# Performance work log

Hardware: AMD Instinct MI355X
Metric: run time of the kernel (lower is better)

## Reference

```python
import jax, jax.numpy as jnp
import numpy as np

NUM_GROUPS = 8
MEAN_DEGREE = 32.0
MAX_NUM_ITER = 10
NUM_NODES = 50000
NUM_UND_EDGES = 800000


def setup_inputs() -> dict:
    key = jax.random.key(0)
    k1, k2, k3, k4 = jax.random.split(key, 4)
    src = jax.random.randint(k1, (NUM_UND_EDGES,), 0, NUM_NODES)
    dst = jax.random.randint(k2, (NUM_UND_EDGES,), 0, NUM_NODES)
    # symmetric directed edge list: reverse of directed edge e (< M) is e + M
    edge_index = jnp.stack([jnp.concatenate([src, dst]), jnp.concatenate([dst, src])])  # [2, 2M]
    E = 2 * NUM_UND_EDGES
    edge_attr = jnp.ones((E,), jnp.float32)
    # _init_messages: messages / marginals initialized near uniform 1/q, normalized
    msg = jax.random.uniform(k3, (E, NUM_GROUPS), jnp.float32, 0.5, 1.5)
    message_init = msg / msg.sum(-1, keepdims=True)
    psi = jax.random.uniform(k4, (NUM_NODES, NUM_GROUPS), jnp.float32, 0.5, 1.5)
    psi_init = psi / psi.sum(-1, keepdims=True)
    # beta = log(q / (sqrt(c) - 1) + 1) per __init__
    beta = jnp.float32(np.log(NUM_GROUPS / (np.sqrt(MEAN_DEGREE) - 1.0) + 1.0))
    return {"edge_index": edge_index, "edge_attr": edge_attr,
            "message_init": message_init, "psi_init": psi_init,
            "beta": beta, "num_nodes": NUM_NODES}


def _bp(edge_index, edge_attr, message_init, psi_init, beta, num_nodes):
    E = edge_index.shape[1]
    M = E // 2
    src_n, dst_n = edge_index[0], edge_index[1]
    rev = jnp.concatenate([jnp.arange(M) + M, jnp.arange(M)])  # reverse directed edge
    ones = jnp.ones((E,), message_init.dtype)
    deg = jax.ops.segment_sum(ones, dst_n, num_segments=num_nodes)  # [N]

    def field_of(psi):
        # approximate BP external field h_k = -(beta/N) * sum_i d_i psi_i(k)
        return -(beta / num_nodes) * (deg[:, None] * psi).sum(0)  # [q]

    def step(carry, _):
        msg, psi, h = carry
        # per-edge factor (1 + psi_{k->i}(t) * (e^{beta w} - 1)); log-domain product
        ew = jnp.exp(beta * edge_attr) - 1.0                       # [E]
        log_src = jnp.log1p(msg * ew[:, None])                     # [E, q]
        node_logprod = jax.ops.segment_sum(log_src, dst_n, num_segments=num_nodes)  # [N, q]
        # message i->j: field * prod over incoming k->i except j->i (divide-out reverse edge)
        new_msg = jnp.exp(h[None, :] + node_logprod[src_n] - log_src[rev])
        new_msg = new_msg / new_msg.sum(-1, keepdims=True)
        new_psi = jnp.exp(h[None, :] + node_logprod)
        new_psi = new_psi / new_psi.sum(-1, keepdims=True)
        diff = jnp.max(jnp.abs(new_msg - msg))
        return (new_msg, new_psi, field_of(new_psi)), diff

    h0 = field_of(psi_init)
    (msg, psi, _), diffs = jax.lax.scan(step, (message_init, psi_init, h0), None, length=MAX_NUM_ITER)
    return msg, psi, diffs


def reference(edge_index, edge_attr, message_init, psi_init, beta, num_nodes):
    msg, psi, diffs = _bp(edge_index, edge_attr, message_init, psi_init, beta, num_nodes)
    # module returns (message_map, marginal_psi, csc_map); csc_map is an index cache, omitted
    return (msg, psi)
```

## Files before the change

### kernel.cpp

```cpp
#include <hip/hip_runtime.h>


constexpr int Q = 8;
constexpr int NITER = 10;
constexpr int TB = 256;
constexpr int TBW = 512;
constexpr int WPB = TBW / 64;
constexpr int MAXDEG = 128;
constexpr int NSTRIPE = 64;

__global__ void pass1_kernel(const int* __restrict__ dst, int* __restrict__ count,
                             int* __restrict__ p_local, int E) {
    int e = blockIdx.x * TB + threadIdx.x;
    if (e < E) p_local[e] = atomicAdd(&count[dst[e]], 1);
}

__global__ void scan_kernel(const int* __restrict__ count, int* __restrict__ row_start, int N) {
    __shared__ int sums[1024];
    int tid = threadIdx.x;
    int chunk = (N + 1023) >> 10;
    int lo = min(tid * chunk, N), hi = min(lo + chunk, N);
    int s = 0;
    for (int i = lo; i < hi; ++i) s += count[i];
    sums[tid] = s;
    __syncthreads();
    for (int off = 1; off < 1024; off <<= 1) {
        int add = (tid >= off) ? sums[tid - off] : 0;
        __syncthreads();
        sums[tid] += add;
        __syncthreads();
    }
    int run = (tid > 0) ? sums[tid - 1] : 0;
    for (int i = lo; i < hi; ++i) { row_start[i] = run; run += count[i]; }
    if (tid == 1023) row_start[N] = sums[1023];
}

__global__ void aux_kernel(const int* __restrict__ src, const int* __restrict__ dst,
                           const int* __restrict__ p_local,
                           const int* __restrict__ row_start,
                           const float* __restrict__ edge_attr,
                           const float* __restrict__ beta_p,
                           const float* __restrict__ msg_init,
                           int4* __restrict__ aux4,
                           float* __restrict__ mt0,
                           int E, int M) {
    int e = blockIdx.x * TB + threadIdx.x;
    if (e >= E) return;
    int re = (e < M) ? (e + M) : (e - M);
    float beta = *beta_p;
    float w  = expf(beta * edge_attr[e])  - 1.0f;
    float wr = expf(beta * edge_attr[re]) - 1.0f;
    int p  = row_start[dst[e]] + p_local[e];
    int rp = row_start[src[e]] + p_local[re];
    aux4[p] = make_int4(rp, __float_as_int(wr), e, 0);
    const float4* mp = reinterpret_cast<const float4*>(msg_init + (size_t)e * Q);
    float4 m0 = mp[0], m1 = mp[1];
    float4* op = reinterpret_cast<float4*>(mt0 + (size_t)p * Q);
    op[0] = make_float4(m0.x * w, m0.y * w, m0.z * w, m0.w * w);
    op[1] = make_float4(m1.x * w, m1.y * w, m1.z * w, m1.w * w);
}

__global__ void field_kernel(const float* __restrict__ psi,
                             const int* __restrict__ row_start,
                             float* __restrict__ hacc, int N) {
    int t = blockIdx.x * TB + threadIdx.x;
    int n = t >> 3, k = t & 7;
    float contrib = 0.f;
    if (n < N)
        contrib = (float)(row_start[n + 1] - row_start[n]) * psi[(size_t)n * Q + k];
    contrib += __shfl_xor(contrib, 8);
    contrib += __shfl_xor(contrib, 16);
    contrib += __shfl_xor(contrib, 32);
    if ((threadIdx.x & 63) < Q)
        atomicAdd(&hacc[(blockIdx.x & (NSTRIPE - 1)) * Q + (threadIdx.x & 7)], contrib);
}

__global__ void h_fin_kernel(const float* __restrict__ beta_p, float* __restrict__ h,
                             float* __restrict__ hacc, float invN) {
    float s = 0.f;
    if (threadIdx.x < Q)
        for (int j = threadIdx.x; j < NSTRIPE * Q; j += Q) s += hacc[j];
    __syncthreads();
    if (threadIdx.x < Q) h[threadIdx.x] = -(*beta_p) * invN * s;
    for (int j = threadIdx.x; j < NSTRIPE * Q; j += TB) hacc[j] = 0.f;
}

template <bool FINAL>
__global__ __launch_bounds__(TBW) void bp_iter_kernel(
    const float* __restrict__ mt_old,
    const int4*  __restrict__ aux4,
    const int*   __restrict__ row_start,
    const float* __restrict__ h,
    float* __restrict__ out,
    float* __restrict__ psi_out,
    float* __restrict__ hacc,
    int N, int M) {
    __shared__ float lbuf[WPB][MAXDEG * Q];
    __shared__ float accQ[Q];
    int tid = threadIdx.x;
    if (tid < Q) accQ[tid] = 0.f;
    __syncthreads();
    int wave = tid >> 6, lane = tid & 63, es = lane >> 3, k = lane & 7;
    int n = blockIdx.x * WPB + wave;
    float contrib = 0.f;
    if (n < N) {
        int lo = row_start[n], hi = row_start[n + 1];
        float acc = 0.f;
        for (int i = lo + es; i < hi; i += 8) {
            float l = log1pf(mt_old[(size_t)i * Q + k]);
            int idx = i - lo;
            if (idx < MAXDEG) lbuf[wave][idx * Q + k] = l;
            acc += l;
        }
        acc += __shfl_xor(acc, 8);
        acc += __shfl_xor(acc, 16);
        acc += __shfl_xor(acc, 32);
        float nlp = h[k] + acc;
        float pp = expf(nlp);
        float s = pp;
        s += __shfl_xor(s, 1);
        s += __shfl_xor(s, 2);
        s += __shfl_xor(s, 4);
        pp /= s;
        if (lane < Q) {
            psi_out[(size_t)n * Q + k] = pp;
            contrib = (float)(hi - lo) * pp;
        }
        for (int i = lo + es; i < hi; i += 8) {
            int idx = i - lo;
            float l = (idx < MAXDEG) ? lbuf[wave][idx * Q + k]
                                     : log1pf(mt_old[(size_t)i * Q + k]);
            float t = expf(nlp - l);
            float ss = t;
            ss += __shfl_xor(ss, 1);
            ss += __shfl_xor(ss, 2);
            ss += __shfl_xor(ss, 4);
            float inv = 1.0f / ss;
            int4 a = aux4[i];
            if (FINAL) {
                int e = a.z;
                int oe = (e < M) ? (e + M) : (e - M);
                out[(size_t)oe * Q + k] = t * inv;
            } else {
                out[(size_t)a.x * Q + k] = t * inv * __int_as_float(a.y);
            }
        }
        if (lane < Q) atomicAdd(&accQ[k], contrib);
    }
    __syncthreads();
    if (tid < Q)
        atomicAdd(&hacc[(blockIdx.x & (NSTRIPE - 1)) * Q + tid], accQ[tid]);
}

extern "C" void kernel_launch(void* const* d_in, const int* in_sizes, int n_in,
                              void* d_out, int out_size, void* d_ws, size_t ws_size,
                              hipStream_t stream) {
    const int*   edge_index = (const int*)d_in[0];
    const float* edge_attr  = (const float*)d_in[1];
    const float* msg_init   = (const float*)d_in[2];
    const float* psi_init   = (const float*)d_in[3];
    const float* beta_p     = (const float*)d_in[4];

    const int E = in_sizes[1];
    const int M = E / 2;
    const int N = in_sizes[3] / Q;

    const int* src = edge_index;
    const int* dst = edge_index + E;

    float* out_msg = (float*)d_out;
    float* out_psi = (float*)d_out + (size_t)E * Q;

    char* ws = (char*)d_ws;
    size_t off = 0;
    auto alloc = [&](size_t bytes) -> void* {
        void* p = (void*)(ws + off);
        off = (off + bytes + 255) & ~(size_t)255;
        return p;
    };
    float* bufA      = (float*)alloc((size_t)E * Q * sizeof(float));
    int4*  aux4      = (int4*)alloc((size_t)E * sizeof(int4));
    int*   p_local   = (int*)alloc((size_t)E * sizeof(int));
    int*   row_start = (int*)alloc((size_t)(N + 1) * sizeof(int));
    float* h         = (float*)alloc(Q * sizeof(float));
    float* hacc      = (float*)alloc(NSTRIPE * Q * sizeof(float));
    int*   count     = (int*)bufA;
    (void)ws_size;

    const int gE   = (E + TB - 1) / TB;
    const int gOct = (N * Q + TB - 1) / TB;
    const int gF   = (N + WPB - 1) / WPB;
    const float invN = 1.0f / (float)N;

    hipMemsetAsync(count, 0, (size_t)N * sizeof(int), stream);
    hipMemsetAsync(hacc, 0, NSTRIPE * Q * sizeof(float), stream);
    pass1_kernel<<<gE, TB, 0, stream>>>(dst, count, p_local, E);
    scan_kernel<<<1, 1024, 0, stream>>>(count, row_start, N);
    aux_kernel<<<gE, TB, 0, stream>>>(src, dst, p_local, row_start, edge_attr,
                                      beta_p, msg_init, aux4, out_msg, E, M);
    field_kernel<<<gOct, TB, 0, stream>>>(psi_init, row_start, hacc, N);
    h_fin_kernel<<<1, TB, 0, stream>>>(beta_p, h, hacc, invN);

    const float* cur = out_msg;
    float*       alt = bufA;
    for (int t = 0; t < NITER - 1; ++t) {
        bp_iter_kernel<false><<<gF, TBW, 0, stream>>>(cur, aux4, row_start, h,
                                                      alt, out_psi, hacc, N, M);
        h_fin_kernel<<<1, TB, 0, stream>>>(beta_p, h, hacc, invN);
        float* tmp = (float*)cur; cur = alt; alt = tmp;
    }
    bp_iter_kernel<true><<<gF, TBW, 0, stream>>>(cur, aux4, row_start, h,
                                                 out_msg, out_psi, hacc, N, M);
}
```

Baseline: 1.017 ms.

## Fold field finalization into BP iteration kernel and streamline setup kernels

```diff
diff --git a/kernel.cpp b/kernel.cpp
--- a/kernel.cpp
+++ b/kernel.cpp
@@ -6,13 +6,14 @@
 constexpr int TB = 256;
 constexpr int TBW = 512;
 constexpr int WPB = TBW / 64;
-constexpr int MAXDEG = 128;
+constexpr int MAXDEG = 64;
 constexpr int NSTRIPE = 64;
+constexpr int CSTRIDE = 16;
 
 __global__ void pass1_kernel(const int* __restrict__ dst, int* __restrict__ count,
                              int* __restrict__ p_local, int E) {
     int e = blockIdx.x * TB + threadIdx.x;
-    if (e < E) p_local[e] = atomicAdd(&count[dst[e]], 1);
+    if (e < E) p_local[e] = atomicAdd(&count[(size_t)dst[e] * CSTRIDE], 1);
 }
 
 __global__ void scan_kernel(const int* __restrict__ count, int* __restrict__ row_start, int N) {
@@ -21,7 +22,7 @@
     int chunk = (N + 1023) >> 10;
     int lo = min(tid * chunk, N), hi = min(lo + chunk, N);
     int s = 0;
-    for (int i = lo; i < hi; ++i) s += count[i];
+    for (int i = lo; i < hi; ++i) s += count[(size_t)i * CSTRIDE];
     sums[tid] = s;
     __syncthreads();
     for (int off = 1; off < 1024; off <<= 1) {
@@ -31,11 +32,12 @@
         __syncthreads();
     }
     int run = (tid > 0) ? sums[tid - 1] : 0;
-    for (int i = lo; i < hi; ++i) { row_start[i] = run; run += count[i]; }
+    for (int i = lo; i < hi; ++i) { row_start[i] = run; run += count[(size_t)i * CSTRIDE]; }
     if (tid == 1023) row_start[N] = sums[1023];
 }
 
-__global__ void aux_kernel(const int* __restrict__ src, const int* __restrict__ dst,
+__global__ void aux_kernel(const int* __restrict__ src_row,
+                           const int* __restrict__ dst_row,
                            const int* __restrict__ p_local,
                            const int* __restrict__ row_start,
                            const float* __restrict__ edge_attr,
@@ -43,26 +45,32 @@
                            const float* __restrict__ msg_init,
                            int4* __restrict__ aux4,
                            float* __restrict__ mt0,
-                           int E, int M) {
+                           int M) {
     int e = blockIdx.x * TB + threadIdx.x;
-    if (e >= E) return;
-    int re = (e < M) ? (e + M) : (e - M);
+    if (e >= M) return;
+    int s0 = src_row[e], d0 = dst_row[e];
     float beta = *beta_p;
-    float w  = expf(beta * edge_attr[e])  - 1.0f;
-    float wr = expf(beta * edge_attr[re]) - 1.0f;
-    int p  = row_start[dst[e]] + p_local[e];
-    int rp = row_start[src[e]] + p_local[re];
-    aux4[p] = make_int4(rp, __float_as_int(wr), e, 0);
+    float w  = expf(beta * edge_attr[e])     - 1.0f;
+    float wr = expf(beta * edge_attr[e + M]) - 1.0f;
+    int p  = row_start[d0] + p_local[e];
+    int rp = row_start[s0] + p_local[e + M];
+    aux4[p]  = make_int4(rp, __float_as_int(wr), e, 0);
+    aux4[rp] = make_int4(p,  __float_as_int(w),  e + M, 0);
     const float4* mp = reinterpret_cast<const float4*>(msg_init + (size_t)e * Q);
     float4 m0 = mp[0], m1 = mp[1];
     float4* op = reinterpret_cast<float4*>(mt0 + (size_t)p * Q);
     op[0] = make_float4(m0.x * w, m0.y * w, m0.z * w, m0.w * w);
     op[1] = make_float4(m1.x * w, m1.y * w, m1.z * w, m1.w * w);
+    const float4* mq = reinterpret_cast<const float4*>(msg_init + (size_t)(e + M) * Q);
+    float4 r0 = mq[0], r1 = mq[1];
+    float4* oq = reinterpret_cast<float4*>(mt0 + (size_t)rp * Q);
+    oq[0] = make_float4(r0.x * wr, r0.y * wr, r0.z * wr, r0.w * wr);
+    oq[1] = make_float4(r1.x * wr, r1.y * wr, r1.z * wr, r1.w * wr);
 }
 
 __global__ void field_kernel(const float* __restrict__ psi,
                              const int* __restrict__ row_start,
-                             float* __restrict__ hacc, int N) {
+                             float* __restrict__ hacc0, int N) {
     int t = blockIdx.x * TB + threadIdx.x;
     int n = t >> 3, k = t & 7;
     float contrib = 0.f;
@@ -72,17 +80,7 @@
     contrib += __shfl_xor(contrib, 16);
     contrib += __shfl_xor(contrib, 32);
     if ((threadIdx.x & 63) < Q)
-        atomicAdd(&hacc[(blockIdx.x & (NSTRIPE - 1)) * Q + (threadIdx.x & 7)], contrib);
-}
-
-__global__ void h_fin_kernel(const float* __restrict__ beta_p, float* __restrict__ h,
-                             float* __restrict__ hacc, float invN) {
-    float s = 0.f;
-    if (threadIdx.x < Q)
-        for (int j = threadIdx.x; j < NSTRIPE * Q; j += Q) s += hacc[j];
-    __syncthreads();
-    if (threadIdx.x < Q) h[threadIdx.x] = -(*beta_p) * invN * s;
-    for (int j = threadIdx.x; j < NSTRIPE * Q; j += TB) hacc[j] = 0.f;
+        atomicAdd(&hacc0[(blockIdx.x & (NSTRIPE - 1)) * Q + (threadIdx.x & 7)], contrib);
 }
 
 template <bool FINAL>
@@ -90,32 +88,51 @@
     const float* __restrict__ mt_old,
     const int4*  __restrict__ aux4,
     const int*   __restrict__ row_start,
-    const float* __restrict__ h,
+    const float* __restrict__ beta_p,
+    const float* __restrict__ hacc_cur,
+    float* __restrict__ hacc_nxt,
+    float* __restrict__ hacc_zer,
     float* __restrict__ out,
     float* __restrict__ psi_out,
-    float* __restrict__ hacc,
-    int N, int M) {
+    int N, int M, float invN) {
     __shared__ float lbuf[WPB][MAXDEG * Q];
+    __shared__ int4  auxbuf[WPB][MAXDEG];
+    __shared__ float hpart[WPB][Q];
     __shared__ float accQ[Q];
     int tid = threadIdx.x;
+    int wave = tid >> 6, lane = tid & 63, es = lane >> 3, k = lane & 7;
+
+    float v = hacc_cur[tid];
+    v += __shfl_xor(v, 8);
+    v += __shfl_xor(v, 16);
+    v += __shfl_xor(v, 32);
+    if (lane < Q) hpart[wave][lane] = v;
     if (tid < Q) accQ[tid] = 0.f;
+    if (blockIdx.x == 0) hacc_zer[tid] = 0.f;
     __syncthreads();
-    int wave = tid >> 6, lane = tid & 63, es = lane >> 3, k = lane & 7;
+    float beta = *beta_p;
+    float hk = 0.f;
+#pragma unroll
+    for (int w2 = 0; w2 < WPB; ++w2) hk += hpart[w2][k];
+    hk *= -beta * invN;
+
     int n = blockIdx.x * WPB + wave;
     float contrib = 0.f;
     if (n < N) {
         int lo = row_start[n], hi = row_start[n + 1];
         float acc = 0.f;
         for (int i = lo + es; i < hi; i += 8) {
-            float l = log1pf(mt_old[(size_t)i * Q + k]);
             int idx = i - lo;
+            float mtv = mt_old[(size_t)i * Q + k];
+            if (k == 0 && idx < MAXDEG) auxbuf[wave][idx] = aux4[i];
+            float l = log1pf(mtv);
             if (idx < MAXDEG) lbuf[wave][idx * Q + k] = l;
             acc += l;
         }
         acc += __shfl_xor(acc, 8);
         acc += __shfl_xor(acc, 16);
         acc += __shfl_xor(acc, 32);
-        float nlp = h[k] + acc;
+        float nlp = hk + acc;
         float pp = expf(nlp);
         float s = pp;
         s += __shfl_xor(s, 1);
@@ -123,7 +140,7 @@
         s += __shfl_xor(s, 4);
         pp /= s;
         if (lane < Q) {
-            psi_out[(size_t)n * Q + k] = pp;
+            if (FINAL) psi_out[(size_t)n * Q + k] = pp;
             contrib = (float)(hi - lo) * pp;
         }
         for (int i = lo + es; i < hi; i += 8) {
@@ -136,10 +153,9 @@
             ss += __shfl_xor(ss, 2);
             ss += __shfl_xor(ss, 4);
             float inv = 1.0f / ss;
-            int4 a = aux4[i];
+            int4 a = (idx < MAXDEG) ? auxbuf[wave][idx] : aux4[i];
             if (FINAL) {
-                int e = a.z;
-                int oe = (e < M) ? (e + M) : (e - M);
+                int oe = (a.z < M) ? (a.z + M) : (a.z - M);
                 out[(size_t)oe * Q + k] = t * inv;
             } else {
                 out[(size_t)a.x * Q + k] = t * inv * __int_as_float(a.y);
@@ -149,7 +165,7 @@
     }
     __syncthreads();
     if (tid < Q)
-        atomicAdd(&hacc[(blockIdx.x & (NSTRIPE - 1)) * Q + tid], accQ[tid]);
+        atomicAdd(&hacc_nxt[(blockIdx.x & (NSTRIPE - 1)) * Q + tid], accQ[tid]);
 }
 
 extern "C" void kernel_launch(void* const* d_in, const int* in_sizes, int n_in,
@@ -181,34 +197,43 @@
     float* bufA      = (float*)alloc((size_t)E * Q * sizeof(float));
     int4*  aux4      = (int4*)alloc((size_t)E * sizeof(int4));
     int*   p_local   = (int*)alloc((size_t)E * sizeof(int));
+    int*   count     = (int*)alloc((size_t)N * CSTRIDE * sizeof(int));
     int*   row_start = (int*)alloc((size_t)(N + 1) * sizeof(int));
-    float* h         = (float*)alloc(Q * sizeof(float));
-    float* hacc      = (float*)alloc(NSTRIPE * Q * sizeof(float));
-    int*   count     = (int*)bufA;
+    float* hacc3     = (float*)alloc(3 * NSTRIPE * Q * sizeof(float));
     (void)ws_size;
 
     const int gE   = (E + TB - 1) / TB;
+    const int gM   = (M + TB - 1) / TB;
     const int gOct = (N * Q + TB - 1) / TB;
     const int gF   = (N + WPB - 1) / WPB;
     const float invN = 1.0f / (float)N;
 
-    hipMemsetAsync(count, 0, (size_t)N * sizeof(int), stream);
-    hipMemsetAsync(hacc, 0, NSTRIPE * Q * sizeof(float), stream);
+    hipMemsetAsync(count, 0, (size_t)N * CSTRIDE * sizeof(int), stream);
+    hipMemsetAsync(hacc3, 0, 3 * NSTRIPE * Q * sizeof(float), stream);
     pass1_kernel<<<gE, TB, 0, stream>>>(dst, count, p_local, E);
     scan_kernel<<<1, 1024, 0, stream>>>(count, row_start, N);
-    aux_kernel<<<gE, TB, 0, stream>>>(src, dst, p_local, row_start, edge_attr,
-                                      beta_p, msg_init, aux4, out_msg, E, M);
-    field_kernel<<<gOct, TB, 0, stream>>>(psi_init, row_start, hacc, N);
-    h_fin_kernel<<<1, TB, 0, stream>>>(beta_p, h, hacc, invN);
+    aux_kernel<<<gM, TB, 0, stream>>>(src, dst, p_local, row_start, edge_attr,
+                                      beta_p, msg_init, aux4, out_msg, M);
+    field_kernel<<<gOct, TB, 0, stream>>>(psi_init, row_start, hacc3, N);
 
     const float* cur = out_msg;
     float*       alt = bufA;
     for (int t = 0; t < NITER - 1; ++t) {
-        bp_iter_kernel<false><<<gF, TBW, 0, stream>>>(cur, aux4, row_start, h,
-                                                      alt, out_psi, hacc, N, M);
-        h_fin_kernel<<<1, TB, 0, stream>>>(beta_p, h, hacc, invN);
+        bp_iter_kernel<false><<<gF, TBW, 0, stream>>>(
+            cur, aux4, row_start, beta_p,
+            hacc3 + (size_t)(t % 3) * NSTRIPE * Q,
+            hacc3 + (size_t)((t + 1) % 3) * NSTRIPE * Q,
+            hacc3 + (size_t)((t + 2) % 3) * NSTRIPE * Q,
+            alt, out_psi, N, M, invN);
         float* tmp = (float*)cur; cur = alt; alt = tmp;
     }
-    bp_iter_kernel<true><<<gF, TBW, 0, stream>>>(cur, aux4, row_start, h,
-                                                 out_msg, out_psi, hacc, N, M);
-}
+    {
+        int t = NITER - 1;
+        bp_iter_kernel<true><<<gF, TBW, 0, stream>>>(
+            cur, aux4, row_start, beta_p,
+            hacc3 + (size_t)(t % 3) * NSTRIPE * Q,
+            hacc3 + (size_t)((t + 1) % 3) * NSTRIPE * Q,
+            hacc3 + (size_t)((t + 2) % 3) * NSTRIPE * Q,
+            out_msg, out_psi, N, M, invN);
+    }
+}
```

After: 951.8 us. -6.4%, faster.
